# Kernel tuning notes

Measured on AMD Instinct MI355X. Metric: run time of the kernel, lower is better.

## Reference

```python
import jax, jax.numpy as jnp
import numpy as np

T, B, V, L_MAX = 1000, 64, 1024, 64
BLANK = 0
LAMBDA_FAIR = 0.5
NUM_GROUPS = 2
NEG = jnp.float32(-1e30)  # finite stand-in for -inf (nan-safe under vjp)


def setup_inputs() -> dict:
    key = jax.random.key(0)
    k1, k2, k3, k4, k5 = jax.random.split(key, 5)
    # caller passes log-softmaxed acoustic model outputs [T, B, V]
    log_probs = jax.nn.log_softmax(jax.random.normal(k1, (T, B, V), jnp.float32), axis=-1)
    # flat concatenated targets; values in [1, V) (blank=0 excluded, as in real CTC targets)
    targets = jax.random.randint(k2, (B * L_MAX,), 1, V, dtype=jnp.int32)
    input_lengths = jax.random.randint(k3, (B,), T // 2, T + 1, dtype=jnp.int32)
    target_lengths = jax.random.randint(k4, (B,), 0, L_MAX, dtype=jnp.int32)  # 0 allowed (tests t_len==0 branch)
    group_ids = jax.random.randint(k5, (B,), 0, NUM_GROUPS, dtype=jnp.int32)
    return {"log_probs": log_probs, "targets": targets, "input_lengths": input_lengths,
            "target_lengths": target_lengths, "group_ids": group_ids}


def _ctc_per_sample(log_probs, targets, input_lengths, target_lengths):
    """Batched CTC NLL (reduction='none'), log-domain alpha recursion."""
    Tn, Bn, Vn = log_probs.shape
    # unflatten targets per sample: offsets = exclusive cumsum of target_lengths
    offsets = jnp.cumsum(target_lengths) - target_lengths                      # [B]
    pos = offsets[:, None] + jnp.arange(L_MAX)[None, :]                        # [B, L]
    valid = jnp.arange(L_MAX)[None, :] < target_lengths[:, None]
    tgt = jnp.where(valid, targets[jnp.clip(pos, 0, targets.shape[0] - 1)], BLANK)  # [B, L]

    S = 2 * L_MAX + 1  # extended label sequence with interleaved blanks
    ext = jnp.full((Bn, S), BLANK, dtype=targets.dtype).at[:, 1::2].set(tgt)   # [B, S]
    # emission log-probs gathered once: em[t, b, s] = log_probs[t, b, ext[b, s]]
    em = jnp.take_along_axis(log_probs, jnp.broadcast_to(ext[None], (Tn, Bn, S)), axis=2)

    ext_m2 = jnp.pad(ext[:, :-2], ((0, 0), (2, 0)), constant_values=BLANK)
    s_idx = jnp.arange(S)
    allow_skip = (s_idx[None, :] >= 2) & (ext != BLANK) & (ext != ext_m2)      # [B, S]

    def end_ll(alpha):
        last = 2 * target_lengths                                              # index of final blank
        a1 = jnp.take_along_axis(alpha, last[:, None], axis=1)[:, 0]
        a2 = jnp.take_along_axis(alpha, jnp.clip(last - 1, 0)[:, None], axis=1)[:, 0]
        return jnp.logaddexp(a1, jnp.where(target_lengths > 0, a2, NEG))

    alpha0 = jnp.full((Bn, S), NEG).at[:, 0].set(em[0, :, 0])
    alpha0 = alpha0.at[:, 1].set(jnp.where(target_lengths > 0, em[0, :, 1], NEG))
    final0 = jnp.where(input_lengths == 1, end_ll(alpha0), NEG)

    def step(carry, xs):
        alpha, final = carry
        em_t, t = xs
        sh1 = jnp.concatenate([jnp.full((Bn, 1), NEG), alpha[:, :-1]], axis=1)
        sh2 = jnp.concatenate([jnp.full((Bn, 2), NEG), alpha[:, :-2]], axis=1)
        alpha = jnp.logaddexp(jnp.logaddexp(alpha, sh1),
                              jnp.where(allow_skip, sh2, NEG)) + em_t
        final = jnp.where(t == input_lengths - 1, end_ll(alpha), final)
        return (alpha, final), None

    (_, final), _ = jax.lax.scan(step, (alpha0, final0), (em[1:], jnp.arange(1, Tn)))
    loss = jnp.where(target_lengths > 0, -final, 0.0)   # t_len==0 -> loss 0 (as in original)
    loss = jnp.where(loss < 1e29, loss, 0.0)            # zero_infinity=True
    return loss


def reference(log_probs, targets, input_lengths, target_lengths, group_ids):
    per_sample = _ctc_per_sample(log_probs, targets, input_lengths, target_lengths)  # [B]
    base_loss = per_sample.mean()
    ones = jnp.ones_like(per_sample)
    counts = jax.ops.segment_sum(ones, group_ids, num_segments=NUM_GROUPS)
    sums = jax.ops.segment_sum(per_sample, group_ids, num_segments=NUM_GROUPS)
    group_means = sums / jnp.maximum(counts, 1.0)
    fairness_penalty = jnp.var(group_means, ddof=1)     # torch .var() is unbiased
    total = base_loss + LAMBDA_FAIR * fairness_penalty
    return total, base_loss, fairness_penalty
```

## Files before the change

kernel.cpp:

```cpp
#include <hip/hip_runtime.h>

#define T_ 1000
#define B_ 64
#define V_ 1024
#define LMAX_ 64
#define NEGF (-1e30f)
#define LOG2E_ 1.4426950408889634f
#define LN2_ 0.6931471805599453f
#define P0C 1.4405f
#define P1C (-0.64178f)
#define P2C 0.20128f

__device__ __forceinline__ float ex2(float x) { return __builtin_amdgcn_exp2f(x); }
__device__ __forceinline__ float lg2(float x) { return __builtin_amdgcn_logf(x); }
__device__ __forceinline__ float rlane(float x, int l) {
    return __int_as_float(__builtin_amdgcn_readlane(__float_as_int(x), l));
}
#define FENCE_ __builtin_amdgcn_sched_barrier(0)

__device__ __forceinline__ void load_tgt(const int* __restrict__ targets,
                                         const int* __restrict__ tlen,
                                         int b, int lane, int& tg, int& L) {
    int tl = tlen[lane];
    L = __shfl(tl, b);
    int v = (lane < b) ? tl : 0;
    for (int off = 32; off; off >>= 1) v += __shfl_xor(v, off);
    tg = (lane < L) ? targets[v + lane] : 0;
}

__global__ __launch_bounds__(64) void ctc_fb_k(const float* __restrict__ lp,
                                               const int* __restrict__ targets,
                                               const int* __restrict__ tlen,
                                               const int* __restrict__ ilen,
                                               float* __restrict__ aw) {
    int blk = blockIdx.x, lane = threadIdx.x;
    bool isFwd = blk < B_;
    int b = isFwd ? blk : blk - B_;
    int tg, L;
    load_tgt(targets, tlen, b, lane, tg, L);
    int Tin = ilen[b], Te = Tin - 1;
    int M = Te >> 1;
    int tgp = __shfl_up(tg, 1);
    bool skip1 = (lane >= 1) && (tg != 0) && (tg != tgp);
    int col = (lane == 63) ? 0 : tg;
    int idx = (b << 10) + col;
    float* awb = aw + b * 256;

    if (isFwd) {
        bool is16 = (lane == 16), is32 = (lane == 32), is48 = (lane == 48);
        float a0 = NEGF, a1 = NEGF;
        auto ldG = [&](int g, float4& S) {
            int t0 = 4 * g;
            int ta = t0 < M ? t0 : M, tb2 = t0 + 1 < M ? t0 + 1 : M;
            int tc = t0 + 2 < M ? t0 + 2 : M, td = t0 + 3 < M ? t0 + 3 : M;
            S.x = (lp + ((size_t)ta << 16))[idx];
            S.y = (lp + ((size_t)tb2 << 16))[idx];
            S.z = (lp + ((size_t)tc << 16))[idx];
            S.w = (lp + ((size_t)td << 16))[idx];
        };
        auto shr1 = [&](float x) -> float {
            float v15 = rlane(x, 15), v31 = rlane(x, 31), v47 = rlane(x, 47);
            float bval = is16 ? v15 : (is32 ? v31 : (is48 ? v47 : NEGF));
            return __int_as_float(__builtin_amdgcn_update_dpp(
                __float_as_int(bval), __float_as_int(x), 0x111, 0xF, 0xF, false));
        };
        auto step = [&](float xb, float xe) {
            float p1m = shr1(a1);
            float d0 = a0 - p1m;
            float m0 = fmaxf(a0, p1m);
            float u = ex2(-fabsf(d0));
            float h = fmaf(u, P2C, P1C);
            h = fmaf(u, h, P0C);
            float U = fmaf(u, h, m0);
            float na0 = U + xb;
            float w = skip1 ? U : a0;
            float d1 = a1 - w;
            float m1 = fmaxf(a1, w);
            float v = ex2(-fabsf(d1));
            float h1 = fmaf(v, P2C, P1C);
            h1 = fmaf(v, h1, P0C);
            float na1 = fmaf(v, h1, m1 + xe);
            a0 = na0; a1 = na1;
        };
        if (M >= 35) {
            float4 S0, S1, S2, S3, S4, S5, S6, S7;
            ldG(0, S0); ldG(1, S1); ldG(2, S2); ldG(3, S3);
            ldG(4, S4); ldG(5, S5); ldG(6, S6); ldG(7, S7);
            FENCE_;
            {
                float e0 = S0.x * LOG2E_, e1 = S0.y * LOG2E_;
                float e2 = S0.z * LOG2E_, e3 = S0.w * LOG2E_;
                a0 = (lane == 0) ? rlane(e0, 63) : NEGF;
                a1 = (lane == 0 && L > 0) ? e0 : NEGF;
                step(rlane(e1, 63), e1); step(rlane(e2, 63), e2); step(rlane(e3, 63), e3);
                ldG(8, S0);
                FENCE_;
            }
#define SUBF_F(S, G) do {                                                      \
            float e0_ = S.x * LOG2E_, e1_ = S.y * LOG2E_;                      \
            float e2_ = S.z * LOG2E_, e3_ = S.w * LOG2E_;                      \
            float b0_ = rlane(e0_, 63), b1_ = rlane(e1_, 63);                  \
            float b2_ = rlane(e2_, 63), b3_ = rlane(e3_, 63);                  \
            step(b0_, e0_); step(b1_, e1_); step(b2_, e2_); step(b3_, e3_);    \
            ldG((G) + 8, S);                                                   \
            FENCE_;                                                            \
        } while (0)
            SUBF_F(S1, 1); SUBF_F(S2, 2); SUBF_F(S3, 3); SUBF_F(S4, 4);
            SUBF_F(S5, 5); SUBF_F(S6, 6); SUBF_F(S7, 7);
            int c = 1;
            for (; 32 * c + 31 <= M; ++c) {
                int g0 = 8 * c;
                SUBF_F(S0, g0 + 0); SUBF_F(S1, g0 + 1); SUBF_F(S2, g0 + 2); SUBF_F(S3, g0 + 3);
                SUBF_F(S4, g0 + 4); SUBF_F(S5, g0 + 5); SUBF_F(S6, g0 + 6); SUBF_F(S7, g0 + 7);
            }
#undef SUBF_F
            int tb = 32 * c;
#define SUBT_F(S, T0) do {                                                     \
            float e0_ = S.x * LOG2E_, e1_ = S.y * LOG2E_;                      \
            float e2_ = S.z * LOG2E_, e3_ = S.w * LOG2E_;                      \
            float b0_ = rlane(e0_, 63), b1_ = rlane(e1_, 63);                  \
            float b2_ = rlane(e2_, 63), b3_ = rlane(e3_, 63);                  \
            if ((T0) + 0 <= M) step(b0_, e0_);                                 \
            if ((T0) + 1 <= M) step(b1_, e1_);                                 \
            if ((T0) + 2 <= M) step(b2_, e2_);                                 \
            if ((T0) + 3 <= M) step(b3_, e3_);                                 \
        } while (0)
            SUBT_F(S0, tb + 0);  SUBT_F(S1, tb + 4);  SUBT_F(S2, tb + 8);  SUBT_F(S3, tb + 12);
            SUBT_F(S4, tb + 16); SUBT_F(S5, tb + 20); SUBT_F(S6, tb + 24); SUBT_F(S7, tb + 28);
#undef SUBT_F
        } else {
            float e = lp[idx] * LOG2E_;
            a0 = (lane == 0) ? rlane(e, 63) : NEGF;
            a1 = (lane == 0 && L > 0) ? e : NEGF;
            for (int t = 1; t <= M; ++t) {
                float xe = (lp + ((size_t)t << 16))[idx] * LOG2E_;
                step(rlane(xe, 63), xe);
            }
        }
        awb[lane] = a0;
        awb[64 + lane] = a1;
    } else {
        bool is15 = (lane == 15), is31 = (lane == 31), is47 = (lane == 47);
        int K = Te - M;
        float B0 = (lane == L) ? 0.0f : NEGF;
        float B1 = (L > 0 && lane == L - 1) ? 0.0f : NEGF;
        auto ldG = [&](int g, float4& S) {
            int t0 = Te - 4 * g;
            int ta = t0 > 0 ? t0 : 0, tb2 = t0 - 1 > 0 ? t0 - 1 : 0;
            int tc = t0 - 2 > 0 ? t0 - 2 : 0, td = t0 - 3 > 0 ? t0 - 3 : 0;
            S.x = (lp + ((size_t)ta << 16))[idx];
            S.y = (lp + ((size_t)tb2 << 16))[idx];
            S.z = (lp + ((size_t)tc << 16))[idx];
            S.w = (lp + ((size_t)td << 16))[idx];
        };
        auto shl1 = [&](float x) -> float {
            float v16 = rlane(x, 16), v32 = rlane(x, 32), v48 = rlane(x, 48);
            float bval = is15 ? v16 : (is31 ? v32 : (is47 ? v48 : NEGF));
            return __int_as_float(__builtin_amdgcn_update_dpp(
                __float_as_int(bval), __float_as_int(x), 0x101, 0xF, 0xF, false));
        };
        auto stepb = [&](float xb, float xe) {
            float z = B1 + xe;
            float t0v = B0 + xb;
            float d0 = t0v - z;
            float m0 = fmaxf(t0v, z);
            float u = ex2(-fabsf(d0));
            float h = fmaf(u, P2C, P1C);
            h = fmaf(u, h, P0C);
            float B0n = fmaf(u, h, m0);
            float y = skip1 ? B0n : t0v;
            float arg = shl1(y);
            float d1 = z - arg;
            float m1 = fmaxf(z, arg);
            float v = ex2(-fabsf(d1));
            float h1 = fmaf(v, P2C, P1C);
            h1 = fmaf(v, h1, P0C);
            float B1n = fmaf(v, h1, m1);
            B0 = B0n; B1 = B1n;
        };
        if (K >= 35) {
            float4 S0, S1, S2, S3, S4, S5, S6, S7;
            ldG(0, S0); ldG(1, S1); ldG(2, S2); ldG(3, S3);
            ldG(4, S4); ldG(5, S5); ldG(6, S6); ldG(7, S7);
            FENCE_;
#define SUBF_B(S, G) do {                                                      \
            float e0_ = S.x * LOG2E_, e1_ = S.y * LOG2E_;                      \
            float e2_ = S.z * LOG2E_, e3_ = S.w * LOG2E_;                      \
            float b0_ = rlane(e0_, 63), b1_ = rlane(e1_, 63);                  \
            float b2_ = rlane(e2_, 63), b3_ = rlane(e3_, 63);                  \
            stepb(b0_, e0_); stepb(b1_, e1_); stepb(b2_, e2_); stepb(b3_, e3_);\
            ldG((G) + 8, S);                                                   \
            FENCE_;                                                            \
        } while (0)
            SUBF_B(S0, 0); SUBF_B(S1, 1); SUBF_B(S2, 2); SUBF_B(S3, 3);
            SUBF_B(S4, 4); SUBF_B(S5, 5); SUBF_B(S6, 6); SUBF_B(S7, 7);
            int c = 1;
            for (; 32 * c + 31 <= K - 1; ++c) {
                int g0 = 8 * c;
                SUBF_B(S0, g0 + 0); SUBF_B(S1, g0 + 1); SUBF_B(S2, g0 + 2); SUBF_B(S3, g0 + 3);
                SUBF_B(S4, g0 + 4); SUBF_B(S5, g0 + 5); SUBF_B(S6, g0 + 6); SUBF_B(S7, g0 + 7);
            }
#undef SUBF_B
            int kb = 32 * c;
#define SUBT_B(S, K0) do {                                                     \
            float e0_ = S.x * LOG2E_, e1_ = S.y * LOG2E_;                      \
            float e2_ = S.z * LOG2E_, e3_ = S.w * LOG2E_;                      \
            float b0_ = rlane(e0_, 63), b1_ = rlane(e1_, 63);                  \
            float b2_ = rlane(e2_, 63), b3_ = rlane(e3_, 63);                  \
            if ((K0) + 0 <= K - 1) stepb(b0_, e0_);                            \
            if ((K0) + 1 <= K - 1) stepb(b1_, e1_);                            \
            if ((K0) + 2 <= K - 1) stepb(b2_, e2_);                            \
            if ((K0) + 3 <= K - 1) stepb(b3_, e3_);                            \
        } while (0)
            SUBT_B(S0, kb + 0);  SUBT_B(S1, kb + 4);  SUBT_B(S2, kb + 8);  SUBT_B(S3, kb + 12);
            SUBT_B(S4, kb + 16); SUBT_B(S5, kb + 20); SUBT_B(S6, kb + 24); SUBT_B(S7, kb + 28);
#undef SUBT_B
        } else {
            for (int k = 0; k < K; ++k) {
                int t = Te - k;
                float xe = (lp + ((size_t)t << 16))[idx] * LOG2E_;
                stepb(rlane(xe, 63), xe);
            }
        }
        awb[128 + lane] = B0;
        awb[192 + lane] = B1;
    }
}

__global__ __launch_bounds__(64) void combine_k(const float* __restrict__ aw,
                                                const int* __restrict__ tlen,
                                                const int* __restrict__ ilen,
                                                float* __restrict__ losses) {
    int b = blockIdx.x, lane = threadIdx.x;
    const float* awb = aw + b * 256;
    float s0 = awb[lane] + awb[128 + lane];
    float s1 = awb[64 + lane] + awb[192 + lane];
    float m = fmaxf(s0, s1);
    for (int off = 32; off; off >>= 1) m = fmaxf(m, __shfl_xor(m, off));
    float sum = ex2(s0 - m) + ex2(s1 - m);
    for (int off = 32; off; off >>= 1) sum += __shfl_xor(sum, off);
    if (lane == 0) {
        int L = tlen[b];
        float fin = lg2(sum) + m;
        if (ilen[b] <= 0) fin = NEGF;
        float loss = (L > 0) ? -fin * LN2_ : 0.0f;
        if (!(loss < 1e29f)) loss = 0.0f;
        losses[b] = loss;
    }
}

__global__ __launch_bounds__(64) void ctc_rec_direct_k(const float* __restrict__ lp,
                                                       const int* __restrict__ targets,
                                                       const int* __restrict__ tlen,
                                                       const int* __restrict__ ilen,
                                                       float* __restrict__ losses) {
    int b = blockIdx.x, lane = threadIdx.x;
    int tg, L;
    load_tgt(targets, tlen, b, lane, tg, L);
    int Tin = ilen[b], Te = Tin - 1;
    int tgp = __shfl_up(tg, 1);
    bool skip1 = (lane >= 1) && (tg != 0) && (tg != tgp);
    bool is16 = (lane == 16), is32 = (lane == 32), is48 = (lane == 48);
    int col = (lane == 63) ? 0 : tg;
    int idx = (b << 10) + col;
    float a0 = NEGF, a1 = NEGF;
    auto shr1 = [&](float x) -> float {
        float v15 = rlane(x, 15), v31 = rlane(x, 31), v47 = rlane(x, 47);
        float bval = is16 ? v15 : (is32 ? v31 : (is48 ? v47 : NEGF));
        return __int_as_float(__builtin_amdgcn_update_dpp(
            __float_as_int(bval), __float_as_int(x), 0x111, 0xF, 0xF, false));
    };
    auto step = [&](float xb, float xe) {
        float p1m = shr1(a1);
        float d0 = a0 - p1m;
        float m0 = fmaxf(a0, p1m);
        float u = ex2(-fabsf(d0));
        float h = fmaf(u, P2C, P1C);
        h = fmaf(u, h, P0C);
        float U = fmaf(u, h, m0);
        float na0 = U + xb;
        float w = skip1 ? U : a0;
        float d1 = a1 - w;
        float m1 = fmaxf(a1, w);
        float v = ex2(-fabsf(d1));
        float h1 = fmaf(v, P2C, P1C);
        h1 = fmaf(v, h1, P0C);
        float na1 = fmaf(v, h1, m1 + xe);
        a0 = na0; a1 = na1;
    };
    if (Tin >= 1) {
        float e = lp[idx] * LOG2E_;
        a0 = (lane == 0) ? rlane(e, 63) : NEGF;
        a1 = (lane == 0 && L > 0) ? e : NEGF;
        for (int t = 1; t <= Te; ++t) {
            float xe = (lp + ((size_t)t << 16))[idx] * LOG2E_;
            step(rlane(xe, 63), xe);
        }
    }
    int lidx = (L > 0) ? (L - 1) : 0;
    float aPrev = __shfl(a1, lidx);
    float aLast = __shfl(a0, (L < 63) ? L : 63);
    float x = aLast, y = (L > 0) ? aPrev : NEGF;
    float m = fmaxf(x, y), d = fminf(x, y) - m;
    float fin = m + lg2(1.0f + ex2(d));
    if (Tin <= 0) fin = NEGF;
    if (lane == 0) {
        float loss = (L > 0) ? -fin * LN2_ : 0.0f;
        if (!(loss < 1e29f)) loss = 0.0f;
        losses[b] = loss;
    }
}

__global__ __launch_bounds__(64) void finalize_k(const float* __restrict__ losses,
                                                 const int* __restrict__ gid,
                                                 float* __restrict__ out) {
    int lane = threadIdx.x;
    float l = losses[lane];
    int g = gid[lane];
    float s = l;
    float s0 = (g == 0) ? l : 0.0f, c0 = (g == 0) ? 1.0f : 0.0f;
    float s1 = (g == 1) ? l : 0.0f, c1 = (g == 1) ? 1.0f : 0.0f;
    for (int off = 32; off; off >>= 1) {
        s  += __shfl_xor(s, off);
        s0 += __shfl_xor(s0, off);
        c0 += __shfl_xor(c0, off);
        s1 += __shfl_xor(s1, off);
        c1 += __shfl_xor(c1, off);
    }
    if (lane == 0) {
        float base = s * (1.0f / B_);
        float m0 = s0 / fmaxf(c0, 1.0f);
        float m1 = s1 / fmaxf(c1, 1.0f);
        float mean = 0.5f * (m0 + m1);
        float var = (m0 - mean) * (m0 - mean) + (m1 - mean) * (m1 - mean);
        out[0] = base + 0.5f * var;
        out[1] = base;
        out[2] = var;
    }
}

extern "C" void kernel_launch(void* const* d_in, const int* in_sizes, int n_in,
                              void* d_out, int out_size, void* d_ws, size_t ws_size,
                              hipStream_t stream) {
    const float* lp = (const float*)d_in[0];
    const int* targets = (const int*)d_in[1];
    const int* ilen = (const int*)d_in[2];
    const int* tlen = (const int*)d_in[3];
    const int* gid = (const int*)d_in[4];
    float* out = (float*)d_out;

    char* ws = (char*)d_ws;
    float* losses = (float*)ws;
    float* aw = (float*)(ws + 1024);
    size_t need = 1024 + (size_t)B_ * 256 * 4;

    if (ws_size >= need) {
        ctc_fb_k<<<2 * B_, 64, 0, stream>>>(lp, targets, tlen, ilen, aw);
        combine_k<<<B_, 64, 0, stream>>>(aw, tlen, ilen, losses);
    } else {
        ctc_rec_direct_k<<<B_, 64, 0, stream>>>(lp, targets, tlen, ilen, losses);
    }
    finalize_k<<<1, 64, 0, stream>>>(losses, gid, out);
}
```

Baseline: 46.37 us.

## Use quadratic log1p-exp approximation and fuse combine with finalize kernel

Swaps the cubic polynomial for log2(1+2^-x) in every forward and backward recursion step for a quadratic one, saving one FMA on the serial critical path of each step. It also merges the per-sample combine kernel and the group-statistics finalize kernel into a single 256-thread block, removing one kernel launch. The lower-order approximation is less accurate in the log-sum-exp and can shift the loss values. It also adds a guard on the short forward path for zero-length inputs.

```diff
diff --git a/kernel.cpp b/kernel.cpp
--- a/kernel.cpp
+++ b/kernel.cpp
@@ -3,13 +3,11 @@
 #define T_ 1000
 #define B_ 64
 #define V_ 1024
-#define LMAX_ 64
 #define NEGF (-1e30f)
 #define LOG2E_ 1.4426950408889634f
 #define LN2_ 0.6931471805599453f
-#define P0C 1.4405f
-#define P1C (-0.64178f)
-#define P2C 0.20128f
+#define C1Q 1.385f
+#define C2Q (-0.385f)
 
 __device__ __forceinline__ float ex2(float x) { return __builtin_amdgcn_exp2f(x); }
 __device__ __forceinline__ float lg2(float x) { return __builtin_amdgcn_logf(x); }
@@ -69,16 +67,14 @@
             float d0 = a0 - p1m;
             float m0 = fmaxf(a0, p1m);
             float u = ex2(-fabsf(d0));
-            float h = fmaf(u, P2C, P1C);
-            h = fmaf(u, h, P0C);
+            float h = fmaf(u, C2Q, C1Q);
             float U = fmaf(u, h, m0);
             float na0 = U + xb;
             float w = skip1 ? U : a0;
             float d1 = a1 - w;
             float m1 = fmaxf(a1, w);
             float v = ex2(-fabsf(d1));
-            float h1 = fmaf(v, P2C, P1C);
-            h1 = fmaf(v, h1, P0C);
+            float h1 = fmaf(v, C2Q, C1Q);
             float na1 = fmaf(v, h1, m1 + xe);
             a0 = na0; a1 = na1;
         };
@@ -128,7 +124,7 @@
             SUBT_F(S0, tb + 0);  SUBT_F(S1, tb + 4);  SUBT_F(S2, tb + 8);  SUBT_F(S3, tb + 12);
             SUBT_F(S4, tb + 16); SUBT_F(S5, tb + 20); SUBT_F(S6, tb + 24); SUBT_F(S7, tb + 28);
 #undef SUBT_F
-        } else {
+        } else if (Tin >= 1) {
             float e = lp[idx] * LOG2E_;
             a0 = (lane == 0) ? rlane(e, 63) : NEGF;
             a1 = (lane == 0 && L > 0) ? e : NEGF;
@@ -165,16 +161,14 @@
             float d0 = t0v - z;
             float m0 = fmaxf(t0v, z);
             float u = ex2(-fabsf(d0));
-            float h = fmaf(u, P2C, P1C);
-            h = fmaf(u, h, P0C);
+            float h = fmaf(u, C2Q, C1Q);
             float B0n = fmaf(u, h, m0);
             float y = skip1 ? B0n : t0v;
             float arg = shl1(y);
             float d1 = z - arg;
             float m1 = fmaxf(z, arg);
             float v = ex2(-fabsf(d1));
-            float h1 = fmaf(v, P2C, P1C);
-            h1 = fmaf(v, h1, P0C);
+            float h1 = fmaf(v, C2Q, C1Q);
             float B1n = fmaf(v, h1, m1);
             B0 = B0n; B1 = B1n;
         };
@@ -227,25 +221,55 @@
     }
 }
 
-__global__ __launch_bounds__(64) void combine_k(const float* __restrict__ aw,
-                                                const int* __restrict__ tlen,
-                                                const int* __restrict__ ilen,
-                                                float* __restrict__ losses) {
-    int b = blockIdx.x, lane = threadIdx.x;
-    const float* awb = aw + b * 256;
-    float s0 = awb[lane] + awb[128 + lane];
-    float s1 = awb[64 + lane] + awb[192 + lane];
-    float m = fmaxf(s0, s1);
-    for (int off = 32; off; off >>= 1) m = fmaxf(m, __shfl_xor(m, off));
-    float sum = ex2(s0 - m) + ex2(s1 - m);
-    for (int off = 32; off; off >>= 1) sum += __shfl_xor(sum, off);
-    if (lane == 0) {
-        int L = tlen[b];
-        float fin = lg2(sum) + m;
-        if (ilen[b] <= 0) fin = NEGF;
-        float loss = (L > 0) ? -fin * LN2_ : 0.0f;
-        if (!(loss < 1e29f)) loss = 0.0f;
-        losses[b] = loss;
+__global__ __launch_bounds__(256) void tail_k(const float* __restrict__ aw,
+                                              const int* __restrict__ tlen,
+                                              const int* __restrict__ ilen,
+                                              const int* __restrict__ gid,
+                                              float* __restrict__ out) {
+    __shared__ float lossS[B_];
+    int tid = threadIdx.x, w = tid >> 6, lane = tid & 63;
+    for (int j = 0; j < 16; ++j) {
+        int b = w * 16 + j;
+        const float* awb = aw + b * 256;
+        float s0 = awb[lane] + awb[128 + lane];
+        float s1 = awb[64 + lane] + awb[192 + lane];
+        float m = fmaxf(s0, s1);
+        for (int off = 32; off; off >>= 1) m = fmaxf(m, __shfl_xor(m, off));
+        float sum = ex2(s0 - m) + ex2(s1 - m);
+        for (int off = 32; off; off >>= 1) sum += __shfl_xor(sum, off);
+        if (lane == 0) {
+            int L = tlen[b];
+            float fin = lg2(sum) + m;
+            if (ilen[b] <= 0) fin = NEGF;
+            float loss = (L > 0) ? -fin * LN2_ : 0.0f;
+            if (!(loss < 1e29f)) loss = 0.0f;
+            lossS[b] = loss;
+        }
+    }
+    __syncthreads();
+    if (w == 0) {
+        float l = lossS[lane];
+        int g = gid[lane];
+        float s = l;
+        float s0 = (g == 0) ? l : 0.0f, c0 = (g == 0) ? 1.0f : 0.0f;
+        float s1 = (g == 1) ? l : 0.0f, c1 = (g == 1) ? 1.0f : 0.0f;
+        for (int off = 32; off; off >>= 1) {
+            s  += __shfl_xor(s, off);
+            s0 += __shfl_xor(s0, off);
+            c0 += __shfl_xor(c0, off);
+            s1 += __shfl_xor(s1, off);
+            c1 += __shfl_xor(c1, off);
+        }
+        if (lane == 0) {
+            float base = s * (1.0f / B_);
+            float m0 = s0 / fmaxf(c0, 1.0f);
+            float m1 = s1 / fmaxf(c1, 1.0f);
+            float mean = 0.5f * (m0 + m1);
+            float var = (m0 - mean) * (m0 - mean) + (m1 - mean) * (m1 - mean);
+            out[0] = base + 0.5f * var;
+            out[1] = base;
+            out[2] = var;
+        }
     }
 }
 
@@ -275,16 +299,14 @@
         float d0 = a0 - p1m;
         float m0 = fmaxf(a0, p1m);
         float u = ex2(-fabsf(d0));
-        float h = fmaf(u, P2C, P1C);
-        h = fmaf(u, h, P0C);
+        float h = fmaf(u, C2Q, C1Q);
         float U = fmaf(u, h, m0);
         float na0 = U + xb;
         float w = skip1 ? U : a0;
         float d1 = a1 - w;
         float m1 = fmaxf(a1, w);
         float v = ex2(-fabsf(d1));
-        float h1 = fmaf(v, P2C, P1C);
-        h1 = fmaf(v, h1, P0C);
+        float h1 = fmaf(v, C2Q, C1Q);
         float na1 = fmaf(v, h1, m1 + xe);
         a0 = na0; a1 = na1;
     };
@@ -356,9 +378,9 @@
 
     if (ws_size >= need) {
         ctc_fb_k<<<2 * B_, 64, 0, stream>>>(lp, targets, tlen, ilen, aw);
-        combine_k<<<B_, 64, 0, stream>>>(aw, tlen, ilen, losses);
+        tail_k<<<1, 256, 0, stream>>>(aw, tlen, ilen, gid, out);
     } else {
         ctc_rec_direct_k<<<B_, 64, 0, stream>>>(lp, targets, tlen, ilen, losses);
-    }
-    finalize_k<<<1, 64, 0, stream>>>(losses, gid, out);
-}
+        finalize_k<<<1, 64, 0, stream>>>(losses, gid, out);
+    }
+}
```

Measured after the change: 55.19 us. 19.0% more time.
